# Optimization experiments

Hardware: AMD Instinct MI355X
Metric: run time of the kernel (lower is better)

Reference implementation:

```python
import jax, jax.numpy as jnp
import numpy as np

N_NODES = 100000


def gcn_conv(x, W, b, src, dst, num_nodes):
    # PyG GCNConv: add self-loops, symmetric deg^-1/2 normalization,
    # linear transform, scatter-add aggregation at dst, then bias.
    loop = jnp.arange(num_nodes, dtype=src.dtype)
    row = jnp.concatenate([src, loop])  # message sources
    col = jnp.concatenate([dst, loop])  # message destinations
    deg = jax.ops.segment_sum(jnp.ones_like(col, dtype=x.dtype), col,
                              num_segments=num_nodes)
    dinv = jnp.where(deg > 0, jax.lax.rsqrt(deg), 0.0)
    norm = dinv[row] * dinv[col]  # [E+N]
    h = x @ W  # [N, out]
    msg = h[row] * norm[:, None]  # gather + scale, [E+N, out]
    out = jax.ops.segment_sum(msg, col, num_segments=num_nodes)  # scatter-add
    return out + b


def setup_inputs() -> dict:
    key = jax.random.key(0)
    k1, k2, k3, k4, k5, k6 = jax.random.split(key, 6)
    dim_in, dim_h = 256, 128
    E = 1600000
    x = jax.random.normal(k1, (N_NODES, dim_in), dtype=jnp.float32)
    edge_index = jax.random.randint(k2, (2, E), 0, N_NODES, dtype=jnp.int64)
    # Glorot-style init for GCNConv weights
    W1 = jax.random.normal(k3, (dim_in, dim_h), dtype=jnp.float32) * (1.0 / np.sqrt(dim_in))
    b1 = jnp.zeros((dim_h,), dtype=jnp.float32)
    W2 = jax.random.normal(k4, (dim_h, 1), dtype=jnp.float32) * (1.0 / np.sqrt(dim_h))
    b2 = jnp.zeros((1,), dtype=jnp.float32)
    return {"x": x, "edge_index": edge_index, "W1": W1, "b1": b1, "W2": W2, "b2": b2}


def reference(x, edge_index, W1, b1, W2, b2):
    src, dst = edge_index[0], edge_index[1]
    h = gcn_conv(x, W1, b1, src, dst, N_NODES)
    h = jax.nn.relu(h)
    h = gcn_conv(h, W2, b2, src, dst, N_NODES)
    return jax.nn.sigmoid(h)  # [N, 1]
```

## Files before the change

kernel.cpp:

```cpp
#include <hip/hip_runtime.h>
#include <math.h>

#define NN 100000
#define DIN 256
#define DH 128
#define GEMM_NB 1563
#define BSHIFT 9
#define BNODES 512
#define NB_BUCKET 196
#define BCAP 12288
#define PA_EDGES 8192

using short8  = __attribute__((ext_vector_type(8))) short;
using float4v = __attribute__((ext_vector_type(4))) float;

static __device__ __forceinline__ unsigned short f2bf(float f) {
    unsigned u = __float_as_uint(f);
    unsigned r = u + 0x7fffu + ((u >> 16) & 1u);
    return (unsigned short)(r >> 16);
}
static __device__ __forceinline__ float bf_lo(unsigned u) { return __uint_as_float(u << 16); }
static __device__ __forceinline__ float bf_hi(unsigned u) { return __uint_as_float(u & 0xffff0000u); }

__global__ __launch_bounds__(256) void k_prepW(const float* __restrict__ W1,
                                               unsigned short* __restrict__ W1p) {
    int t = blockIdx.x * 256 + threadIdx.x;
    int lane = t & 63;
    int ks   = (t >> 6) & 7;
    int nt   = (t >> 9) & 1;
    int wv   = (t >> 10) & 3;
    int n = wv * 32 + nt * 16 + (lane & 15);
    int kbase = ks * 32 + (lane >> 4) * 8;
    short8 v;
#pragma unroll
    for (int j = 0; j < 8; ++j) v[j] = (short)f2bf(W1[(kbase + j) * DH + n]);
    *(short8*)&W1p[(long long)t * 8] = v;
}

__global__ __launch_bounds__(256) void k_gemm(const float* __restrict__ x,
                                              const unsigned short* __restrict__ W1p,
                                              unsigned short* __restrict__ hs) {
    __shared__ unsigned short aL[64 * 32 * 8];
    const int tid  = threadIdx.x;
    const int wave = tid >> 6;
    const int lane = tid & 63;
    const int quad = lane >> 4;
    const int m16  = lane & 15;
    const int row0 = blockIdx.x * 64;

    short8 bfr[2][8];
#pragma unroll
    for (int nt = 0; nt < 2; ++nt)
#pragma unroll
        for (int ks = 0; ks < 8; ++ks)
            bfr[nt][ks] = ((const short8*)W1p)[((wave * 2 + nt) * 8 + ks) * 64 + lane];

#pragma unroll
    for (int it = 0; it < 8; ++it) {
        int id  = it * 256 + tid;
        int row = id >> 5;
        int kb  = id & 31;
        int gr  = row0 + row;
        float4 f0, f1;
        if (gr < NN) {
            const float* xp = &x[(long long)gr * DIN + kb * 8];
            f0 = *(const float4*)xp;
            f1 = *(const float4*)(xp + 4);
        } else {
            f0 = make_float4(0.f, 0.f, 0.f, 0.f);
            f1 = f0;
        }
        short8 v;
        v[0] = (short)f2bf(f0.x); v[1] = (short)f2bf(f0.y);
        v[2] = (short)f2bf(f0.z); v[3] = (short)f2bf(f0.w);
        v[4] = (short)f2bf(f1.x); v[5] = (short)f2bf(f1.y);
        v[6] = (short)f2bf(f1.z); v[7] = (short)f2bf(f1.w);
        int chunk = row * 32 + (kb ^ (row & 31));
        *(short8*)&aL[chunk * 8] = v;
    }
    __syncthreads();

    float4v acc[4][2];
#pragma unroll
    for (int mt = 0; mt < 4; ++mt)
#pragma unroll
        for (int nt = 0; nt < 2; ++nt)
            acc[mt][nt] = (float4v)(0.0f);

#pragma unroll
    for (int mt = 0; mt < 4; ++mt) {
        int row = mt * 16 + m16;
#pragma unroll
        for (int ks = 0; ks < 8; ++ks) {
            int kb = ks * 4 + quad;
            int chunk = row * 32 + (kb ^ (row & 31));
            short8 a = *(const short8*)&aL[chunk * 8];
            acc[mt][0] = __builtin_amdgcn_mfma_f32_16x16x32_bf16(a, bfr[0][ks], acc[mt][0], 0, 0, 0);
            acc[mt][1] = __builtin_amdgcn_mfma_f32_16x16x32_bf16(a, bfr[1][ks], acc[mt][1], 0, 0, 0);
        }
    }

    const int n0 = wave * 32;
#pragma unroll
    for (int mt = 0; mt < 4; ++mt) {
#pragma unroll
        for (int r = 0; r < 4; ++r) {
            int row = row0 + mt * 16 + quad * 4 + r;
            if (row < NN) {
#pragma unroll
                for (int nt = 0; nt < 2; ++nt)
                    hs[(long long)row * DH + n0 + nt * 16 + m16] = f2bf(acc[mt][nt][r]);
            }
        }
    }
}

__global__ __launch_bounds__(512) void k_partA(const int* __restrict__ src,
                                               const int* __restrict__ dst, int E,
                                               int* __restrict__ bucketFill,
                                               int2* __restrict__ bucketArr) {
    __shared__ int aCnt[NB_BUCKET];
    __shared__ int aBase[NB_BUCKET];
    const int tid = threadIdx.x;
    for (int i = tid; i < NB_BUCKET; i += 512) aCnt[i] = 0;
    __syncthreads();
    const int e0   = blockIdx.x * PA_EDGES;
    const int eend = min(e0 + PA_EDGES, E);
    for (int e = e0 + tid; e < eend; e += 512)
        atomicAdd(&aCnt[dst[e] >> BSHIFT], 1);
    __syncthreads();
    for (int i = tid; i < NB_BUCKET; i += 512) {
        int c = aCnt[i];
        aBase[i] = c ? atomicAdd(&bucketFill[i], c) : 0;
        aCnt[i] = 0;
    }
    __syncthreads();
    for (int e = e0 + tid; e < eend; e += 512) {
        int d = dst[e];
        int b = d >> BSHIFT;
        int r = atomicAdd(&aCnt[b], 1);
        bucketArr[(long long)b * BCAP + aBase[b] + r] = make_int2(src[e], d);
    }
}

__global__ __launch_bounds__(512) void k_partB(const int* __restrict__ bucketFill,
                                               const int2* __restrict__ bucketArr,
                                               int* __restrict__ cnt,
                                               int* __restrict__ excl,
                                               float* __restrict__ dinv,
                                               int* __restrict__ eidx) {
    __shared__ int h[BNODES];
    __shared__ int hex[BNODES];
    __shared__ int st[256];
    const int tid   = threadIdx.x;
    const int b     = blockIdx.x;
    const int nbase = b << BSHIFT;
    const int len   = bucketFill[b];
    const long long abase = (long long)b * BCAP;

    if (tid < 256) st[tid] = (tid < b) ? bucketFill[tid] : 0;
    __syncthreads();
    for (int off = 128; off > 0; off >>= 1) {
        if (tid < off) st[tid] += st[tid + off];
        __syncthreads();
    }
    const int gbase = st[0];
    __syncthreads();

    for (int i = tid; i < BNODES; i += 512) h[i] = 0;
    __syncthreads();
    for (int k = tid; k < len; k += 512)
        atomicAdd(&h[bucketArr[abase + k].y - nbase], 1);
    __syncthreads();

    int a0 = 0, a1 = 0;
    if (tid < 256) {
        a0 = h[2 * tid]; a1 = h[2 * tid + 1];
        st[tid] = a0 + a1;
    }
    __syncthreads();
    for (int off = 1; off < 256; off <<= 1) {
        int val = (tid < 256 && tid >= off) ? st[tid - off] : 0;
        __syncthreads();
        if (tid < 256) st[tid] += val;
        __syncthreads();
    }
    if (tid < 256) {
        int prev = (tid > 0) ? st[tid - 1] : 0;
        hex[2 * tid]     = prev;
        hex[2 * tid + 1] = prev + a0;
    }
    __syncthreads();

    for (int i = tid; i < BNODES; i += 512) {
        int n = nbase + i;
        if (n < NN) {
            int c = h[i];
            cnt[n]  = c;
            excl[n] = gbase + hex[i];
            dinv[n] = rsqrtf(1.0f + (float)c);
        }
    }
    for (int i = tid; i < BNODES; i += 512) h[i] = 0;
    __syncthreads();

    for (int k = tid; k < len; k += 512) {
        int2 p = bucketArr[abase + k];
        int li = p.y - nbase;
        int r = atomicAdd(&h[li], 1);
        eidx[gbase + hex[li] + r] = p.x;
    }
}

__global__ __launch_bounds__(256) void k_agg1l2(const int* __restrict__ eidx,
                                                const int* __restrict__ excl,
                                                const int* __restrict__ cnt,
                                                const unsigned* __restrict__ hs2,
                                                const float* __restrict__ dinv,
                                                const float* __restrict__ b1,
                                                const float* __restrict__ W2,
                                                float* __restrict__ zs) {
    int w = (blockIdx.x * 256 + threadIdx.x) >> 6;
    if (w >= NN) return;
    int lane = threadIdx.x & 63;
    int offs = excl[w];
    int c = cnt[w];

    float dw = dinv[w];
    unsigned u = hs2[(long long)w * 64 + lane];
    float ax = dw * bf_lo(u);
    float ay = dw * bf_hi(u);

    int j = 0;
    for (; j + 7 < c; j += 8) {
        int s[8]; float es[8]; unsigned uu[8];
#pragma unroll
        for (int q = 0; q < 8; ++q) s[q] = eidx[offs + j + q];
#pragma unroll
        for (int q = 0; q < 8; ++q) es[q] = dinv[s[q]];
#pragma unroll
        for (int q = 0; q < 8; ++q) uu[q] = hs2[(long long)s[q] * 64 + lane];
#pragma unroll
        for (int q = 0; q < 8; ++q) {
            ax = fmaf(es[q], bf_lo(uu[q]), ax);
            ay = fmaf(es[q], bf_hi(uu[q]), ay);
        }
    }
    for (; j + 1 < c; j += 2) {
        int s0 = eidx[offs + j], s1 = eidx[offs + j + 1];
        float e0 = dinv[s0], e1 = dinv[s1];
        unsigned u0 = hs2[(long long)s0 * 64 + lane];
        unsigned u1 = hs2[(long long)s1 * 64 + lane];
        ax = fmaf(e0, bf_lo(u0), ax); ay = fmaf(e0, bf_hi(u0), ay);
        ax = fmaf(e1, bf_lo(u1), ax); ay = fmaf(e1, bf_hi(u1), ay);
    }
    if (j < c) {
        int s0 = eidx[offs + j];
        float e0 = dinv[s0];
        unsigned u0 = hs2[(long long)s0 * 64 + lane];
        ax = fmaf(e0, bf_lo(u0), ax); ay = fmaf(e0, bf_hi(u0), ay);
    }

    float2 bb = ((const float2*)b1)[lane];
    float2 ww = ((const float2*)W2)[lane];
    float r0 = fmaxf(fmaf(dw, ax, bb.x), 0.0f);
    float r1 = fmaxf(fmaf(dw, ay, bb.y), 0.0f);
    float v = r0 * ww.x + r1 * ww.y;
#pragma unroll
    for (int off = 32; off > 0; off >>= 1) v += __shfl_down(v, off);
    if (lane == 0) zs[w] = v * dw;
}

__global__ void k_agg2_final(const int* __restrict__ eidx,
                             const int* __restrict__ excl,
                             const int* __restrict__ cnt,
                             const float* __restrict__ zs,
                             const float* __restrict__ dinv,
                             const float* __restrict__ b2,
                             float* __restrict__ out) {
    int i = blockIdx.x * 256 + threadIdx.x;
    if (i >= NN) return;
    int offs = excl[i];
    int c = cnt[i];
    float v = zs[i];
    int j = 0;
    for (; j + 3 < c; j += 4) {
        int s0 = eidx[offs + j + 0];
        int s1 = eidx[offs + j + 1];
        int s2 = eidx[offs + j + 2];
        int s3 = eidx[offs + j + 3];
        v += zs[s0] + zs[s1] + zs[s2] + zs[s3];
    }
    for (; j < c; ++j) v += zs[eidx[offs + j]];
    float z = fmaf(dinv[i], v, b2[0]);
    out[i] = 1.0f / (1.0f + __expf(-z));
}

extern "C" void kernel_launch(void* const* d_in, const int* in_sizes, int n_in,
                              void* d_out, int out_size, void* d_ws, size_t ws_size,
                              hipStream_t stream) {
    const float* x  = (const float*)d_in[0];
    const int*   ei = (const int*)d_in[1];
    const float* W1 = (const float*)d_in[2];
    const float* b1 = (const float*)d_in[3];
    const float* W2 = (const float*)d_in[4];
    const float* b2 = (const float*)d_in[5];
    float* out = (float*)d_out;

    const int E = in_sizes[1] / 2;
    const int* src = ei;
    const int* dst = ei + E;

    int* wsi = (int*)d_ws;
    float* dinv       = (float*)wsi;
    int*   cnt        = wsi + NN;
    int*   excl       = cnt + NN;
    float* zs         = (float*)(excl + NN);
    int*   bucketFill = (int*)(zs + NN);
    unsigned short* W1p = (unsigned short*)(bucketFill + 256);
    int*   eidx       = (int*)(W1p + 32768);
    int2*  bucketArr  = (int2*)(eidx + E);
    unsigned short* hs = (unsigned short*)(bucketArr + (long long)NB_BUCKET * BCAP);

    const int nb_nodes = (NN + 255) / 256;
    const int pa_nb = (E + PA_EDGES - 1) / PA_EDGES;

    hipMemsetAsync(bucketFill, 0, NB_BUCKET * sizeof(int), stream);

    k_prepW<<<128, 256, 0, stream>>>(W1, W1p);
    k_partA<<<pa_nb, 512, 0, stream>>>(src, dst, E, bucketFill, bucketArr);
    k_partB<<<NB_BUCKET, 512, 0, stream>>>(bucketFill, bucketArr, cnt, excl, dinv, eidx);
    k_gemm<<<GEMM_NB, 256, 0, stream>>>(x, W1p, hs);

    k_agg1l2<<<(NN * 64 + 255) / 256, 256, 0, stream>>>(eidx, excl, cnt,
                                                        (const unsigned*)hs, dinv, b1, W2, zs);

    k_agg2_final<<<nb_nodes, 256, 0, stream>>>(eidx, excl, cnt, zs, dinv, b2, out);
}
```

Before: 302.8 us.

## Merge independent prep kernels into combined launches and batch edge index loads

Folds W1 packing into the edge partition kernel, and runs bucket CSR construction and the bf16 GEMM as disjoint block ranges of one launch. This cuts launch count and lets independent work overlap. The GEMM moves to 512-thread blocks with one N-tile per wave to fit the merged block size. The layer-1 aggregation now loads 16 edge indices per lane in one coalesced read and broadcasts them with readlane, using scalarized offsets. The risk is that the merged GEMM blocks carry extra shared memory and register pressure from the CSR path, which may lower occupancy.

```diff
diff --git a/kernel.cpp b/kernel.cpp
--- a/kernel.cpp
+++ b/kernel.cpp
@@ -10,6 +10,7 @@
 #define NB_BUCKET 196
 #define BCAP 12288
 #define PA_EDGES 8192
+#define PREP_NB 64
 
 using short8  = __attribute__((ext_vector_type(8))) short;
 using float4v = __attribute__((ext_vector_type(4))) float;
@@ -22,42 +23,144 @@
 static __device__ __forceinline__ float bf_lo(unsigned u) { return __uint_as_float(u << 16); }
 static __device__ __forceinline__ float bf_hi(unsigned u) { return __uint_as_float(u & 0xffff0000u); }
 
-__global__ __launch_bounds__(256) void k_prepW(const float* __restrict__ W1,
-                                               unsigned short* __restrict__ W1p) {
-    int t = blockIdx.x * 256 + threadIdx.x;
-    int lane = t & 63;
-    int ks   = (t >> 6) & 7;
-    int nt   = (t >> 9) & 1;
-    int wv   = (t >> 10) & 3;
-    int n = wv * 32 + nt * 16 + (lane & 15);
-    int kbase = ks * 32 + (lane >> 4) * 8;
-    short8 v;
-#pragma unroll
-    for (int j = 0; j < 8; ++j) v[j] = (short)f2bf(W1[(kbase + j) * DH + n]);
-    *(short8*)&W1p[(long long)t * 8] = v;
-}
-
-__global__ __launch_bounds__(256) void k_gemm(const float* __restrict__ x,
-                                              const unsigned short* __restrict__ W1p,
-                                              unsigned short* __restrict__ hs) {
+__global__ __launch_bounds__(512) void k_prep_partA(const float* __restrict__ W1,
+                                                    unsigned short* __restrict__ W1p,
+                                                    const int* __restrict__ src,
+                                                    const int* __restrict__ dst, int E,
+                                                    int* __restrict__ bucketFill,
+                                                    int2* __restrict__ bucketArr) {
+    __shared__ int aCnt[NB_BUCKET];
+    __shared__ int aBase[NB_BUCKET];
+    const int tid = threadIdx.x;
+
+    if (blockIdx.x < PREP_NB) {
+        int t = blockIdx.x * 512 + tid;
+        int lane = t & 63;
+        int ks   = (t >> 6) & 7;
+        int nt   = (t >> 9) & 1;
+        int wv   = (t >> 10) & 3;
+        int n = wv * 32 + nt * 16 + (lane & 15);
+        int kbase = ks * 32 + (lane >> 4) * 8;
+        short8 v;
+#pragma unroll
+        for (int j = 0; j < 8; ++j) v[j] = (short)f2bf(W1[(kbase + j) * DH + n]);
+        *(short8*)&W1p[(long long)t * 8] = v;
+        return;
+    }
+
+    const int ba = blockIdx.x - PREP_NB;
+    for (int i = tid; i < NB_BUCKET; i += 512) aCnt[i] = 0;
+    __syncthreads();
+    const int e0   = ba * PA_EDGES;
+    const int eend = min(e0 + PA_EDGES, E);
+    for (int e = e0 + tid; e < eend; e += 512)
+        atomicAdd(&aCnt[dst[e] >> BSHIFT], 1);
+    __syncthreads();
+    for (int i = tid; i < NB_BUCKET; i += 512) {
+        int c = aCnt[i];
+        aBase[i] = c ? atomicAdd(&bucketFill[i], c) : 0;
+        aCnt[i] = 0;
+    }
+    __syncthreads();
+    for (int e = e0 + tid; e < eend; e += 512) {
+        int d = dst[e];
+        int b = d >> BSHIFT;
+        int r = atomicAdd(&aCnt[b], 1);
+        bucketArr[(long long)b * BCAP + aBase[b] + r] = make_int2(src[e], d);
+    }
+}
+
+__global__ __launch_bounds__(512) void k_gemm_partB(const float* __restrict__ x,
+                                                    const unsigned short* __restrict__ W1p,
+                                                    unsigned short* __restrict__ hs,
+                                                    const int* __restrict__ bucketFill,
+                                                    const int2* __restrict__ bucketArr,
+                                                    int* __restrict__ cnt,
+                                                    int* __restrict__ excl,
+                                                    float* __restrict__ dinv,
+                                                    int* __restrict__ eidx) {
     __shared__ unsigned short aL[64 * 32 * 8];
-    const int tid  = threadIdx.x;
-    const int wave = tid >> 6;
+    __shared__ int h[BNODES];
+    __shared__ int hex[BNODES];
+    __shared__ int st[256];
+    const int tid = threadIdx.x;
+
+    if (blockIdx.x < NB_BUCKET) {
+        const int b     = blockIdx.x;
+        const int nbase = b << BSHIFT;
+        const int len   = bucketFill[b];
+        const long long abase = (long long)b * BCAP;
+
+        if (tid < 256) st[tid] = (tid < b) ? bucketFill[tid] : 0;
+        __syncthreads();
+        for (int off = 128; off > 0; off >>= 1) {
+            if (tid < off) st[tid] += st[tid + off];
+            __syncthreads();
+        }
+        const int gbase = st[0];
+        __syncthreads();
+
+        for (int i = tid; i < BNODES; i += 512) h[i] = 0;
+        __syncthreads();
+        for (int k = tid; k < len; k += 512)
+            atomicAdd(&h[bucketArr[abase + k].y - nbase], 1);
+        __syncthreads();
+
+        int a0 = 0, a1 = 0;
+        if (tid < 256) {
+            a0 = h[2 * tid]; a1 = h[2 * tid + 1];
+            st[tid] = a0 + a1;
+        }
+        __syncthreads();
+        for (int off = 1; off < 256; off <<= 1) {
+            int val = (tid < 256 && tid >= off) ? st[tid - off] : 0;
+            __syncthreads();
+            if (tid < 256) st[tid] += val;
+            __syncthreads();
+        }
+        if (tid < 256) {
+            int prev = (tid > 0) ? st[tid - 1] : 0;
+            hex[2 * tid]     = prev;
+            hex[2 * tid + 1] = prev + a0;
+        }
+        __syncthreads();
+
+        for (int i = tid; i < BNODES; i += 512) {
+            int n = nbase + i;
+            if (n < NN) {
+                int c = h[i];
+                cnt[n]  = c;
+                excl[n] = gbase + hex[i];
+                dinv[n] = rsqrtf(1.0f + (float)c);
+            }
+        }
+        for (int i = tid; i < BNODES; i += 512) h[i] = 0;
+        __syncthreads();
+
+        for (int k = tid; k < len; k += 512) {
+            int2 p = bucketArr[abase + k];
+            int li = p.y - nbase;
+            int r = atomicAdd(&h[li], 1);
+            eidx[gbase + hex[li] + r] = p.x;
+        }
+        return;
+    }
+
+    const int bid  = blockIdx.x - NB_BUCKET;
+    const int w8   = tid >> 6;
     const int lane = tid & 63;
     const int quad = lane >> 4;
     const int m16  = lane & 15;
-    const int row0 = blockIdx.x * 64;
-
-    short8 bfr[2][8];
-#pragma unroll
-    for (int nt = 0; nt < 2; ++nt)
-#pragma unroll
-        for (int ks = 0; ks < 8; ++ks)
-            bfr[nt][ks] = ((const short8*)W1p)[((wave * 2 + nt) * 8 + ks) * 64 + lane];
-
-#pragma unroll
-    for (int it = 0; it < 8; ++it) {
-        int id  = it * 256 + tid;
+    const int row0 = bid * 64;
+
+    short8 bfr[8];
+#pragma unroll
+    for (int ks = 0; ks < 8; ++ks)
+        bfr[ks] = ((const short8*)W1p)[(w8 * 8 + ks) * 64 + lane];
+
+#pragma unroll
+    for (int it = 0; it < 4; ++it) {
+        int id  = it * 512 + tid;
         int row = id >> 5;
         int kb  = id & 31;
         int gr  = row0 + row;
@@ -80,12 +183,9 @@
     }
     __syncthreads();
 
-    float4v acc[4][2];
-#pragma unroll
-    for (int mt = 0; mt < 4; ++mt)
-#pragma unroll
-        for (int nt = 0; nt < 2; ++nt)
-            acc[mt][nt] = (float4v)(0.0f);
+    float4v acc[4];
+#pragma unroll
+    for (int mt = 0; mt < 4; ++mt) acc[mt] = (float4v)(0.0f);
 
 #pragma unroll
     for (int mt = 0; mt < 4; ++mt) {
@@ -95,120 +195,19 @@
             int kb = ks * 4 + quad;
             int chunk = row * 32 + (kb ^ (row & 31));
             short8 a = *(const short8*)&aL[chunk * 8];
-            acc[mt][0] = __builtin_amdgcn_mfma_f32_16x16x32_bf16(a, bfr[0][ks], acc[mt][0], 0, 0, 0);
-            acc[mt][1] = __builtin_amdgcn_mfma_f32_16x16x32_bf16(a, bfr[1][ks], acc[mt][1], 0, 0, 0);
-        }
-    }
-
-    const int n0 = wave * 32;
+            acc[mt] = __builtin_amdgcn_mfma_f32_16x16x32_bf16(a, bfr[ks], acc[mt], 0, 0, 0);
+        }
+    }
+
+    const int n0 = w8 * 16;
 #pragma unroll
     for (int mt = 0; mt < 4; ++mt) {
 #pragma unroll
         for (int r = 0; r < 4; ++r) {
             int row = row0 + mt * 16 + quad * 4 + r;
-            if (row < NN) {
-#pragma unroll
-                for (int nt = 0; nt < 2; ++nt)
-                    hs[(long long)row * DH + n0 + nt * 16 + m16] = f2bf(acc[mt][nt][r]);
-            }
-        }
-    }
-}
-
-__global__ __launch_bounds__(512) void k_partA(const int* __restrict__ src,
-                                               const int* __restrict__ dst, int E,
-                                               int* __restrict__ bucketFill,
-                                               int2* __restrict__ bucketArr) {
-    __shared__ int aCnt[NB_BUCKET];
-    __shared__ int aBase[NB_BUCKET];
-    const int tid = threadIdx.x;
-    for (int i = tid; i < NB_BUCKET; i += 512) aCnt[i] = 0;
-    __syncthreads();
-    const int e0   = blockIdx.x * PA_EDGES;
-    const int eend = min(e0 + PA_EDGES, E);
-    for (int e = e0 + tid; e < eend; e += 512)
-        atomicAdd(&aCnt[dst[e] >> BSHIFT], 1);
-    __syncthreads();
-    for (int i = tid; i < NB_BUCKET; i += 512) {
-        int c = aCnt[i];
-        aBase[i] = c ? atomicAdd(&bucketFill[i], c) : 0;
-        aCnt[i] = 0;
-    }
-    __syncthreads();
-    for (int e = e0 + tid; e < eend; e += 512) {
-        int d = dst[e];
-        int b = d >> BSHIFT;
-        int r = atomicAdd(&aCnt[b], 1);
-        bucketArr[(long long)b * BCAP + aBase[b] + r] = make_int2(src[e], d);
-    }
-}
-
-__global__ __launch_bounds__(512) void k_partB(const int* __restrict__ bucketFill,
-                                               const int2* __restrict__ bucketArr,
-                                               int* __restrict__ cnt,
-                                               int* __restrict__ excl,
-                                               float* __restrict__ dinv,
-                                               int* __restrict__ eidx) {
-    __shared__ int h[BNODES];
-    __shared__ int hex[BNODES];
-    __shared__ int st[256];
-    const int tid   = threadIdx.x;
-    const int b     = blockIdx.x;
-    const int nbase = b << BSHIFT;
-    const int len   = bucketFill[b];
-    const long long abase = (long long)b * BCAP;
-
-    if (tid < 256) st[tid] = (tid < b) ? bucketFill[tid] : 0;
-    __syncthreads();
-    for (int off = 128; off > 0; off >>= 1) {
-        if (tid < off) st[tid] += st[tid + off];
-        __syncthreads();
-    }
-    const int gbase = st[0];
-    __syncthreads();
-
-    for (int i = tid; i < BNODES; i += 512) h[i] = 0;
-    __syncthreads();
-    for (int k = tid; k < len; k += 512)
-        atomicAdd(&h[bucketArr[abase + k].y - nbase], 1);
-    __syncthreads();
-
-    int a0 = 0, a1 = 0;
-    if (tid < 256) {
-        a0 = h[2 * tid]; a1 = h[2 * tid + 1];
-        st[tid] = a0 + a1;
-    }
-    __syncthreads();
-    for (int off = 1; off < 256; off <<= 1) {
-        int val = (tid < 256 && tid >= off) ? st[tid - off] : 0;
-        __syncthreads();
-        if (tid < 256) st[tid] += val;
-        __syncthreads();
-    }
-    if (tid < 256) {
-        int prev = (tid > 0) ? st[tid - 1] : 0;
-        hex[2 * tid]     = prev;
-        hex[2 * tid + 1] = prev + a0;
-    }
-    __syncthreads();
-
-    for (int i = tid; i < BNODES; i += 512) {
-        int n = nbase + i;
-        if (n < NN) {
-            int c = h[i];
-            cnt[n]  = c;
-            excl[n] = gbase + hex[i];
-            dinv[n] = rsqrtf(1.0f + (float)c);
-        }
-    }
-    for (int i = tid; i < BNODES; i += 512) h[i] = 0;
-    __syncthreads();
-
-    for (int k = tid; k < len; k += 512) {
-        int2 p = bucketArr[abase + k];
-        int li = p.y - nbase;
-        int r = atomicAdd(&h[li], 1);
-        eidx[gbase + hex[li] + r] = p.x;
+            if (row < NN)
+                hs[(long long)row * DH + n0 + m16] = f2bf(acc[mt][r]);
+        }
     }
 }
 
@@ -223,42 +222,31 @@
     int w = (blockIdx.x * 256 + threadIdx.x) >> 6;
     if (w >= NN) return;
     int lane = threadIdx.x & 63;
-    int offs = excl[w];
-    int c = cnt[w];
+    int offs = __builtin_amdgcn_readfirstlane(excl[w]);
+    int c    = __builtin_amdgcn_readfirstlane(cnt[w]);
 
     float dw = dinv[w];
     unsigned u = hs2[(long long)w * 64 + lane];
     float ax = dw * bf_lo(u);
     float ay = dw * bf_hi(u);
 
-    int j = 0;
-    for (; j + 7 < c; j += 8) {
-        int s[8]; float es[8]; unsigned uu[8];
-#pragma unroll
-        for (int q = 0; q < 8; ++q) s[q] = eidx[offs + j + q];
-#pragma unroll
-        for (int q = 0; q < 8; ++q) es[q] = dinv[s[q]];
-#pragma unroll
-        for (int q = 0; q < 8; ++q) uu[q] = hs2[(long long)s[q] * 64 + lane];
-#pragma unroll
-        for (int q = 0; q < 8; ++q) {
+    const int l16 = lane & 15;
+    for (int j = 0; j < c; j += 16) {
+        int rem = c - j; if (rem > 16) rem = 16;
+        int idx = offs + j + ((l16 < rem) ? l16 : 0);
+        int sv = eidx[idx];
+        float es[16]; unsigned uu[16];
+#pragma unroll
+        for (int q = 0; q < 16; ++q) if (q < rem) {
+            int sq = __builtin_amdgcn_readlane(sv, q);
+            es[q] = dinv[sq];
+            uu[q] = hs2[(long long)sq * 64 + lane];
+        }
+#pragma unroll
+        for (int q = 0; q < 16; ++q) if (q < rem) {
             ax = fmaf(es[q], bf_lo(uu[q]), ax);
             ay = fmaf(es[q], bf_hi(uu[q]), ay);
         }
-    }
-    for (; j + 1 < c; j += 2) {
-        int s0 = eidx[offs + j], s1 = eidx[offs + j + 1];
-        float e0 = dinv[s0], e1 = dinv[s1];
-        unsigned u0 = hs2[(long long)s0 * 64 + lane];
-        unsigned u1 = hs2[(long long)s1 * 64 + lane];
-        ax = fmaf(e0, bf_lo(u0), ax); ay = fmaf(e0, bf_hi(u0), ay);
-        ax = fmaf(e1, bf_lo(u1), ax); ay = fmaf(e1, bf_hi(u1), ay);
-    }
-    if (j < c) {
-        int s0 = eidx[offs + j];
-        float e0 = dinv[s0];
-        unsigned u0 = hs2[(long long)s0 * 64 + lane];
-        ax = fmaf(e0, bf_lo(u0), ax); ay = fmaf(e0, bf_hi(u0), ay);
     }
 
     float2 bb = ((const float2*)b1)[lane];
@@ -327,10 +315,10 @@
 
     hipMemsetAsync(bucketFill, 0, NB_BUCKET * sizeof(int), stream);
 
-    k_prepW<<<128, 256, 0, stream>>>(W1, W1p);
-    k_partA<<<pa_nb, 512, 0, stream>>>(src, dst, E, bucketFill, bucketArr);
-    k_partB<<<NB_BUCKET, 512, 0, stream>>>(bucketFill, bucketArr, cnt, excl, dinv, eidx);
-    k_gemm<<<GEMM_NB, 256, 0, stream>>>(x, W1p, hs);
+    k_prep_partA<<<PREP_NB + pa_nb, 512, 0, stream>>>(W1, W1p, src, dst, E,
+                                                      bucketFill, bucketArr);
+    k_gemm_partB<<<NB_BUCKET + GEMM_NB, 512, 0, stream>>>(x, W1p, hs, bucketFill, bucketArr,
+                                                          cnt, excl, dinv, eidx);
 
     k_agg1l2<<<(NN * 64 + 255) / 256, 256, 0, stream>>>(eidx, excl, cnt,
                                                         (const unsigned*)hs, dinv, b1, W2, zs);
```

Result: slower. 325.8 us (+7.6%).
